# Optimization experiments

Measured on AMD Instinct MI355X. Metric: run time of the kernel, lower is better.

Reference implementation:

```python
import jax, jax.numpy as jnp
import numpy as np
from jax.scipy.linalg import solve_triangular
from jax.scipy.special import logsumexp

N, K, D = 131072, 32, 32
LOG_2PI = np.float32(np.log(2.0 * np.pi))


def setup_inputs() -> dict:
    key = jax.random.key(0)
    k1, k2, k3, k4 = jax.random.split(key, 4)
    X = jax.random.normal(k1, (N, D), dtype=jnp.float32)
    means = jax.random.normal(k2, (K, D), dtype=jnp.float32)
    chols = jax.random.normal(k3, (K, D, D), dtype=jnp.float32)
    weights = jax.random.normal(k4, (K,), dtype=jnp.float32) - 1.0  # normal_(-1, 1)
    return {"X": X, "means": means, "chols": chols, "weights": weights, "it": 0}


def _neglog_likelihood(X, means, chols, weights):
    d = X.shape[-1]
    n = X.shape[0]
    eye = jnp.eye(d, dtype=X.dtype)
    # sigmas[k] = chols[k] @ chols[k]^T + I  -> (K, D, D)
    sigmas = jnp.einsum('kij,klj->kil', chols, chols) + eye
    L = jnp.linalg.cholesky(sigmas)                      # (K, D, D)
    # per-cluster Gaussian log-densities for all points, batched
    diff = X[None, :, :] - means[:, None, :]             # (K, N, D)
    y = solve_triangular(L, diff.transpose(0, 2, 1), lower=True)  # (K, D, N)
    maha = jnp.sum(y * y, axis=1)                        # (K, N)
    logdet = 2.0 * jnp.sum(jnp.log(jnp.diagonal(L, axis1=-2, axis2=-1)), axis=-1)  # (K,)
    log_dens = -0.5 * (maha + (logdet + d * LOG_2PI)[:, None])    # (K, N)
    dens = jnp.exp(log_dens)                             # (K, N)
    # sum_{i,j} w_i w_j N_i(x) N_j(x) = (sum_k w_k N_k(x))^2
    numer = jnp.square(weights @ dens)                   # (N,)
    # pairwise normaliser Z_ij = N(mu_i; mu_j, S_i + S_j), all pairs batched
    S_ij = sigmas[:, None] + sigmas[None, :]             # (K, K, D, D)
    L_ij = jnp.linalg.cholesky(S_ij)
    dmu = means[:, None, :] - means[None, :, :]          # (K, K, D)
    y_ij = solve_triangular(L_ij, dmu[..., None], lower=True)[..., 0]  # (K, K, D)
    maha_ij = jnp.sum(y_ij * y_ij, axis=-1)              # (K, K)
    logdet_ij = 2.0 * jnp.sum(jnp.log(jnp.diagonal(L_ij, axis1=-2, axis2=-1)), axis=-1)
    Z_ij = jnp.exp(-0.5 * (maha_ij + logdet_ij + d * LOG_2PI))
    z = jnp.sum((weights[:, None] * weights[None, :]) * Z_ij)
    pdf = numer / z                                      # (N,)
    logp = jnp.log(pdf)                                  # (N,)
    return -(logsumexp(logp, axis=0) / n)


def reference(X, means, chols, weights, it):
    return _neglog_likelihood(X, means, chols, weights)
```

## Files before the change

### kernel.cpp

```cpp
#include <hip/hip_runtime.h>
#include <math.h>

#define NPTS  131072
#define NPTB  1024
#define NPRB  256
#define GRID  (NPTB + NPRB)
#define DLOG2PIF 58.8120661f
#define DLOG2PI  58.81206612467475
#define SHIFT 92.0f
#define NEGHALF_LOG2E -0.72134752044f
#define LOG2E 1.44269504089f

typedef __attribute__((ext_vector_type(8)))  short short8;
typedef __attribute__((ext_vector_type(16))) float f32x16;

static __device__ __forceinline__ unsigned bfh(float f) {
  unsigned u = __float_as_uint(f);
  return (u + 0x7FFFu + ((u >> 16) & 1u)) >> 16;
}
static __device__ __forceinline__ float bfhf(float f) {
  return __uint_as_float(bfh(f) << 16);
}

__global__ __launch_bounds__(256) void setup_kernel(
    const float* __restrict__ means, const float* __restrict__ chols,
    const float* __restrict__ wts,
    uint4* __restrict__ Afrag, float* __restrict__ gbuf,
    float* __restrict__ Kc, float* __restrict__ Sg,
    unsigned* __restrict__ ticket)
{
  const int tid = threadIdx.x, wv = tid >> 6, lane = tid & 63;
  const int r = lane & 31, h = lane >> 5;
  const int k = blockIdx.x*4 + wv;
  __shared__ float SshA[4][1056];
  float* Ssh = SshA[wv];
  if (blockIdx.x == 0 && tid == 0) *ticket = 0u;
  const float* cp = chols + (size_t)k*1024 + r*32;
  float4 fa = *(const float4*)(cp + h*8);
  float4 fb = *(const float4*)(cp + h*8 + 4);
  float4 fc = *(const float4*)(cp + 16 + h*8);
  float4 fd = *(const float4*)(cp + 16 + h*8 + 4);
  float v0[8] = {fa.x,fa.y,fa.z,fa.w,fb.x,fb.y,fb.z,fb.w};
  float v1[8] = {fc.x,fc.y,fc.z,fc.w,fd.x,fd.y,fd.z,fd.w};
  short8 hi0, hi1, lo0, lo1;
  #pragma unroll
  for (int j = 0; j < 8; j++) {
    hi0[j] = (short)bfh(v0[j]);  lo0[j] = (short)bfh(v0[j] - bfhf(v0[j]));
    hi1[j] = (short)bfh(v1[j]);  lo1[j] = (short)bfh(v1[j] - bfhf(v1[j]));
  }
  f32x16 acc = {};
  acc = __builtin_amdgcn_mfma_f32_32x32x16_bf16(hi0, hi0, acc, 0,0,0);
  acc = __builtin_amdgcn_mfma_f32_32x32x16_bf16(hi1, hi1, acc, 0,0,0);
  acc = __builtin_amdgcn_mfma_f32_32x32x16_bf16(hi0, lo0, acc, 0,0,0);
  acc = __builtin_amdgcn_mfma_f32_32x32x16_bf16(hi1, lo1, acc, 0,0,0);
  acc = __builtin_amdgcn_mfma_f32_32x32x16_bf16(lo0, hi0, acc, 0,0,0);
  acc = __builtin_amdgcn_mfma_f32_32x32x16_bf16(lo1, hi1, acc, 0,0,0);
  #pragma unroll
  for (int q = 0; q < 16; q++) {
    int row = (q & 3) + 8*(q >> 2) + 4*h;
    Ssh[row*33 + r] = acc[q] + ((row == r) ? 1.0f : 0.0f);
  }
  float a[32];
  #pragma unroll
  for (int j = 0; j < 32; j++) a[j] = Ssh[r*33 + j];
  float ldsum = 0.0f;
  #pragma unroll
  for (int j = 0; j < 32; j++) {
    float dd = __shfl(a[j], j);
    float inv = rsqrtf(dd);
    float sq = dd * inv;
    ldsum += __logf(sq);
    float l = a[j] * inv;
    #pragma unroll
    for (int e = j+1; e < 32; e++) {
      float le = __shfl(l, e);
      a[e] = (r >= e) ? fmaf(-l, le, a[e]) : a[e];
    }
    a[j] = (r == j) ? sq : ((r > j) ? l : a[j]);
  }
  #pragma unroll
  for (int j = 0; j < 32; j++) Ssh[r*33 + j] = a[j];
  float bv[32];
  #pragma unroll
  for (int d = 0; d < 32; d++) {
    float s0 = (d == r) ? 1.0f : 0.0f, s1 = 0.0f;
    #pragma unroll
    for (int j = 0; j + 1 < d; j += 2) {
      s0 = fmaf(-Ssh[d*33 + j],     bv[j],   s0);
      s1 = fmaf(-Ssh[d*33 + j + 1], bv[j+1], s1);
    }
    if (d & 1) s0 = fmaf(-Ssh[d*33 + (d-1)], bv[d-1], s0);
    bv[d] = __fdividef(s0 + s1, Ssh[d*33 + d]);
  }
  #pragma unroll
  for (int d = 0; d < 32; d++) Ssh[d*33 + r] = bv[d];
  float t0[8], t1[8];
  #pragma unroll
  for (int j = 0; j < 8; j++) {
    t0[j] = Ssh[r*33 + h*8 + j];
    t1[j] = Ssh[r*33 + 16 + h*8 + j];
  }
  uint4 s0 = make_uint4(bfh(t0[0])|(bfh(t0[1])<<16), bfh(t0[2])|(bfh(t0[3])<<16),
                        bfh(t0[4])|(bfh(t0[5])<<16), bfh(t0[6])|(bfh(t0[7])<<16));
  uint4 s1 = make_uint4(bfh(t1[0])|(bfh(t1[1])<<16), bfh(t1[2])|(bfh(t1[3])<<16),
                        bfh(t1[4])|(bfh(t1[5])<<16), bfh(t1[6])|(bfh(t1[7])<<16));
  Afrag[(k*2 + 0)*64 + lane] = s0;
  Afrag[(k*2 + 1)*64 + lane] = s1;
  const float* mk = means + k*32;
  float wr = 0.0f;
  #pragma unroll
  for (int j = 0; j < 32; j++) wr = fmaf(bfhf(Ssh[r*33 + j]), mk[j], wr);
  float c = wr*wr;
  #pragma unroll
  for (int off = 16; off > 0; off >>= 1) c += __shfl_xor(c, off);
  float gd = 0.0f;
  #pragma unroll
  for (int rr = 0; rr < 32; rr++)
    gd = fmaf(bfhf(bv[rr]), __shfl(wr, rr), gd);
  if (h == 0) gbuf[k*32 + r] = 2.0f*gd;
  if (lane == 0) {
    float wk = wts[k];
    float ld2 = 2.0f*ldsum + DLOG2PIF;
    Kc[k] = LOG2E*(SHIFT - 0.5f*ld2 - 0.5f*c) + log2f(fabsf(wk));
    Sg[k] = (wk < 0.0f) ? -1.0f : 1.0f;
  }
}

__global__ __launch_bounds__(256, 4) void work_kernel(
    const float* __restrict__ X, const float* __restrict__ means,
    const float* __restrict__ chols, const float* __restrict__ wts,
    const uint4* __restrict__ Afrag, const float* __restrict__ gbuf,
    const float* __restrict__ Kc, const float* __restrict__ Sg,
    double* __restrict__ zterm, double* __restrict__ partials,
    unsigned* __restrict__ ticket, float* __restrict__ out)
{
  __shared__ __align__(16) char smem[16896];
  __shared__ float K2sh[32], sksh[32];
  __shared__ double redd[4], redz[4];
  __shared__ unsigned lastFlag;
  const int tid = threadIdx.x, wv = tid >> 6, lane = tid & 63;
  const int r = lane & 31, h = lane >> 5;
  if (blockIdx.x < NPTB) {
    uint4* fsh = (uint4*)smem;
    if (tid < 32) { K2sh[tid] = Kc[tid]; sksh[tid] = Sg[tid]; }
    const int n0 = blockIdx.x*128 + wv*32 + r;
    short8 xh0, xh1;
    {
      const float* xp = X + (size_t)n0*32;
      float4 fa = *(const float4*)(xp + h*8);
      float4 fb = *(const float4*)(xp + h*8 + 4);
      float4 fc = *(const float4*)(xp + 16 + h*8);
      float4 fd = *(const float4*)(xp + 16 + h*8 + 4);
      float v0[8] = {fa.x,fa.y,fa.z,fa.w,fb.x,fb.y,fb.z,fb.w};
      float v1[8] = {fc.x,fc.y,fc.z,fc.w,fd.x,fd.y,fd.z,fd.w};
      #pragma unroll
      for (int j = 0; j < 8; j++) { xh0[j] = (short)bfh(v0[j]); xh1[j] = (short)bfh(v1[j]); }
    }
    f32x16 accg = {};
    {
      const float* gp = gbuf + r*32 + h*8;
      float4 ga = *(const float4*)(gp);
      float4 gb = *(const float4*)(gp + 4);
      float4 gc = *(const float4*)(gp + 16);
      float4 gd = *(const float4*)(gp + 20);
      float g0[8] = {ga.x,ga.y,ga.z,ga.w,gb.x,gb.y,gb.z,gb.w};
      float g1[8] = {gc.x,gc.y,gc.z,gc.w,gd.x,gd.y,gd.z,gd.w};
      short8 Gh0, Gl0, Gh1, Gl1;
      #pragma unroll
      for (int j = 0; j < 8; j++) {
        Gh0[j] = (short)bfh(g0[j]); Gl0[j] = (short)bfh(g0[j] - bfhf(g0[j]));
        Gh1[j] = (short)bfh(g1[j]); Gl1[j] = (short)bfh(g1[j] - bfhf(g1[j]));
      }
      accg = __builtin_amdgcn_mfma_f32_32x32x16_bf16(Gh0, xh0, accg, 0,0,0);
      accg = __builtin_amdgcn_mfma_f32_32x32x16_bf16(Gl0, xh0, accg, 0,0,0);
      accg = __builtin_amdgcn_mfma_f32_32x32x16_bf16(Gh1, xh1, accg, 0,0,0);
      accg = __builtin_amdgcn_mfma_f32_32x32x16_bf16(Gl1, xh1, accg, 0,0,0);
    }
    float sF = 0.0f;
    #pragma unroll
    for (int ph = 0; ph < 4; ph++) {
      __syncthreads();
      {
        const uint4* src = Afrag + ph*1024;
        uint4 t0 = src[tid], t1 = src[tid+256], t2 = src[tid+512], t3 = src[tid+768];
        fsh[tid] = t0; fsh[tid+256] = t1; fsh[tid+512] = t2; fsh[tid+768] = t3;
      }
      __syncthreads();
      const short8* cp0 = (const short8*)fsh;
      short8 c0 = cp0[lane], c1 = cp0[64 + lane];
      #pragma unroll
      for (int kk = 0; kk < 8; kk++) {
        short8 nf0, nf1;
        if (kk < 7) {
          const short8* np = (const short8*)(fsh + (kk+1)*128);
          nf0 = np[lane]; nf1 = np[64 + lane];
        }
        const int kidx = ph*8 + kk;
        const float Kk = K2sh[kidx], sk = sksh[kidx];
        f32x16 acc2 = {};
        acc2 = __builtin_amdgcn_mfma_f32_32x32x16_bf16(c0, xh0, acc2, 0,0,0);
        acc2 = __builtin_amdgcn_mfma_f32_32x32x16_bf16(c1, xh1, acc2, 0,0,0);
        float ma = 0.f, mb = 0.f;
        #pragma unroll
        for (int q = 0; q < 8; q++) {
          ma = fmaf(acc2[q],   acc2[q],   ma);
          mb = fmaf(acc2[q+8], acc2[q+8], mb);
        }
        const int qg = (kidx & 3) | (((kidx >> 3) & 3) << 2);
        const int hneed = (kidx >> 2) & 1;
        float m = ma + mb - ((h == hneed) ? accg[qg] : 0.0f);
        m += __shfl_xor(m, 32);
        sF = fmaf(sk, exp2f(fmaf(m, NEGHALF_LOG2E, Kk)), sF);
        c0 = nf0; c1 = nf1;
      }
    }
    double Tp = (double)sF*(double)sF;
    if (lane >= 32) Tp = 0.0;
    #pragma unroll
    for (int off = 32; off > 0; off >>= 1) Tp += __shfl_down(Tp, off);
    if (lane == 0) redd[wv] = Tp;
    __syncthreads();
    if (tid == 0) partials[blockIdx.x] = redd[0] + redd[1] + redd[2] + redd[3];
  } else {
    float* Ssh = (float*)smem + wv*1056;
    const int pid = (blockIdx.x - NPTB)*4 + wv, pi = pid >> 5, pj = pid & 31;
    const float* cpi = chols + (size_t)pi*1024 + r*32;
    const float* cpj = chols + (size_t)pj*1024 + r*32;
    float4 ia = *(const float4*)(cpi + h*8);
    float4 ib = *(const float4*)(cpi + h*8 + 4);
    float4 ic = *(const float4*)(cpi + 16 + h*8);
    float4 id = *(const float4*)(cpi + 16 + h*8 + 4);
    float4 ja = *(const float4*)(cpj + h*8);
    float4 jb = *(const float4*)(cpj + h*8 + 4);
    float4 jc = *(const float4*)(cpj + 16 + h*8);
    float4 jd = *(const float4*)(cpj + 16 + h*8 + 4);
    float vi0[8] = {ia.x,ia.y,ia.z,ia.w,ib.x,ib.y,ib.z,ib.w};
    float vi1[8] = {ic.x,ic.y,ic.z,ic.w,id.x,id.y,id.z,id.w};
    float vj0[8] = {ja.x,ja.y,ja.z,ja.w,jb.x,jb.y,jb.z,jb.w};
    float vj1[8] = {jc.x,jc.y,jc.z,jc.w,jd.x,jd.y,jd.z,jd.w};
    short8 I0h,I0l,I1h,I1l,J0h,J0l,J1h,J1l;
    #pragma unroll
    for (int j = 0; j < 8; j++) {
      I0h[j]=(short)bfh(vi0[j]); I0l[j]=(short)bfh(vi0[j]-bfhf(vi0[j]));
      I1h[j]=(short)bfh(vi1[j]); I1l[j]=(short)bfh(vi1[j]-bfhf(vi1[j]));
      J0h[j]=(short)bfh(vj0[j]); J0l[j]=(short)bfh(vj0[j]-bfhf(vj0[j]));
      J1h[j]=(short)bfh(vj1[j]); J1l[j]=(short)bfh(vj1[j]-bfhf(vj1[j]));
    }
    f32x16 pacc = {};
    pacc = __builtin_amdgcn_mfma_f32_32x32x16_bf16(I0h, I0h, pacc, 0,0,0);
    pacc = __builtin_amdgcn_mfma_f32_32x32x16_bf16(I1h, I1h, pacc, 0,0,0);
    pacc = __builtin_amdgcn_mfma_f32_32x32x16_bf16(I0h, I0l, pacc, 0,0,0);
    pacc = __builtin_amdgcn_mfma_f32_32x32x16_bf16(I1h, I1l, pacc, 0,0,0);
    pacc = __builtin_amdgcn_mfma_f32_32x32x16_bf16(I0l, I0h, pacc, 0,0,0);
    pacc = __builtin_amdgcn_mfma_f32_32x32x16_bf16(I1l, I1h, pacc, 0,0,0);
    pacc = __builtin_amdgcn_mfma_f32_32x32x16_bf16(J0h, J0h, pacc, 0,0,0);
    pacc = __builtin_amdgcn_mfma_f32_32x32x16_bf16(J1h, J1h, pacc, 0,0,0);
    pacc = __builtin_amdgcn_mfma_f32_32x32x16_bf16(J0h, J0l, pacc, 0,0,0);
    pacc = __builtin_amdgcn_mfma_f32_32x32x16_bf16(J1h, J1l, pacc, 0,0,0);
    pacc = __builtin_amdgcn_mfma_f32_32x32x16_bf16(J0l, J0h, pacc, 0,0,0);
    pacc = __builtin_amdgcn_mfma_f32_32x32x16_bf16(J1l, J1h, pacc, 0,0,0);
    #pragma unroll
    for (int q = 0; q < 16; q++) {
      int row = (q & 3) + 8*(q >> 2) + 4*h;
      Ssh[row*33 + r] = pacc[q] + ((row == r) ? 2.0f : 0.0f);
    }
    float a[32];
    #pragma unroll
    for (int j = 0; j < 32; j++) a[j] = Ssh[r*33 + j];
    #pragma unroll
    for (int j = 0; j < 32; j++) {
      float dd = __shfl(a[j], j);
      float inv = __frsqrt_rn(dd);
      float sq = dd * inv;
      float l = a[j] * inv;
      #pragma unroll
      for (int e = j+1; e < 32; e++) {
        float le = __shfl(l, e);
        a[e] = (r >= e) ? fmaf(-l, le, a[e]) : a[e];
      }
      a[j] = (r == j) ? sq : ((r > j) ? l : a[j]);
    }
    float acc2 = means[pi*32 + r] - means[pj*32 + r];
    float maha = 0.0f, ldsum = 0.0f;
    #pragma unroll
    for (int d = 0; d < 32; d++) {
      float dd = __shfl(a[d], d);
      float yd = __shfl(acc2, d) / dd;
      maha = fmaf(yd, yd, maha);
      ldsum += __logf(dd);
      acc2 = (r > d) ? fmaf(-a[d], yd, acc2) : acc2;
    }
    if (lane == 0) {
      double vd = -0.5 * ((double)maha + 2.0*(double)ldsum + DLOG2PI);
      zterm[pid] = (double)wts[pi] * (double)wts[pj] * exp(vd);
    }
  }
  __syncthreads();
  if (tid == 0) {
    __threadfence();
    lastFlag = (atomicAdd(ticket, 1u) == GRID - 1) ? 1u : 0u;
  }
  __syncthreads();
  if (lastFlag) {
    __threadfence();
    double t = 0.0, z = 0.0;
    for (int p = tid; p < NPTB; p += 256) t += partials[p];
    for (int p = tid; p < 1024; p += 256) z += zterm[p];
    #pragma unroll
    for (int off = 32; off > 0; off >>= 1) {
      t += __shfl_down(t, off);
      z += __shfl_down(z, off);
    }
    if (lane == 0) { redd[wv] = t; redz[wv] = z; }
    __syncthreads();
    if (tid == 0) {
      t = redd[0] + redd[1] + redd[2] + redd[3];
      z = redz[0] + redz[1] + redz[2] + redz[3];
      double logT = log(t) - 2.0*(double)SHIFT;
      double logz = log(z);
      out[0] = (float)((logz - logT) / (double)NPTS);
    }
  }
}

extern "C" void kernel_launch(void* const* d_in, const int* in_sizes, int n_in,
                              void* d_out, int out_size, void* d_ws, size_t ws_size,
                              hipStream_t stream) {
  const float* X     = (const float*)d_in[0];
  const float* means = (const float*)d_in[1];
  const float* chols = (const float*)d_in[2];
  const float* wts   = (const float*)d_in[3];
  float* out = (float*)d_out;
  char* ws = (char*)d_ws;
  uint4*    Afrag    = (uint4*)ws;
  float*    gbuf     = (float*)(ws + 65536);
  float*    Kc       = (float*)(ws + 69632);
  float*    Sg       = (float*)(ws + 69760);
  double*   zterm    = (double*)(ws + 69888);
  double*   partials = (double*)(ws + 78080);
  unsigned* ticket   = (unsigned*)(ws + 86272);

  setup_kernel<<<8, 256, 0, stream>>>(means, chols, wts, Afrag, gbuf, Kc, Sg, ticket);
  work_kernel<<<GRID, 256, 0, stream>>>(X, means, chols, wts, Afrag, gbuf, Kc, Sg,
                                        zterm, partials, ticket, out);
}
```

Baseline: 131.5 us.

## Move pairwise normaliser to setup kernel and process two point tiles per wave

```diff
diff --git a/kernel.cpp b/kernel.cpp
--- a/kernel.cpp
+++ b/kernel.cpp
@@ -2,9 +2,9 @@
 #include <math.h>
 
 #define NPTS  131072
-#define NPTB  1024
+#define NPTB  512
 #define NPRB  256
-#define GRID  (NPTB + NPRB)
+#define GRIDW NPTB
 #define DLOG2PIF 58.8120661f
 #define DLOG2PI  58.81206612467475
 #define SHIFT 92.0f
@@ -27,203 +27,106 @@
     const float* __restrict__ wts,
     uint4* __restrict__ Afrag, float* __restrict__ gbuf,
     float* __restrict__ Kc, float* __restrict__ Sg,
-    unsigned* __restrict__ ticket)
+    double* __restrict__ zterm, unsigned* __restrict__ ticket)
 {
   const int tid = threadIdx.x, wv = tid >> 6, lane = tid & 63;
   const int r = lane & 31, h = lane >> 5;
-  const int k = blockIdx.x*4 + wv;
   __shared__ float SshA[4][1056];
   float* Ssh = SshA[wv];
-  if (blockIdx.x == 0 && tid == 0) *ticket = 0u;
-  const float* cp = chols + (size_t)k*1024 + r*32;
-  float4 fa = *(const float4*)(cp + h*8);
-  float4 fb = *(const float4*)(cp + h*8 + 4);
-  float4 fc = *(const float4*)(cp + 16 + h*8);
-  float4 fd = *(const float4*)(cp + 16 + h*8 + 4);
-  float v0[8] = {fa.x,fa.y,fa.z,fa.w,fb.x,fb.y,fb.z,fb.w};
-  float v1[8] = {fc.x,fc.y,fc.z,fc.w,fd.x,fd.y,fd.z,fd.w};
-  short8 hi0, hi1, lo0, lo1;
-  #pragma unroll
-  for (int j = 0; j < 8; j++) {
-    hi0[j] = (short)bfh(v0[j]);  lo0[j] = (short)bfh(v0[j] - bfhf(v0[j]));
-    hi1[j] = (short)bfh(v1[j]);  lo1[j] = (short)bfh(v1[j] - bfhf(v1[j]));
-  }
-  f32x16 acc = {};
-  acc = __builtin_amdgcn_mfma_f32_32x32x16_bf16(hi0, hi0, acc, 0,0,0);
-  acc = __builtin_amdgcn_mfma_f32_32x32x16_bf16(hi1, hi1, acc, 0,0,0);
-  acc = __builtin_amdgcn_mfma_f32_32x32x16_bf16(hi0, lo0, acc, 0,0,0);
-  acc = __builtin_amdgcn_mfma_f32_32x32x16_bf16(hi1, lo1, acc, 0,0,0);
-  acc = __builtin_amdgcn_mfma_f32_32x32x16_bf16(lo0, hi0, acc, 0,0,0);
-  acc = __builtin_amdgcn_mfma_f32_32x32x16_bf16(lo1, hi1, acc, 0,0,0);
-  #pragma unroll
-  for (int q = 0; q < 16; q++) {
-    int row = (q & 3) + 8*(q >> 2) + 4*h;
-    Ssh[row*33 + r] = acc[q] + ((row == r) ? 1.0f : 0.0f);
-  }
-  float a[32];
-  #pragma unroll
-  for (int j = 0; j < 32; j++) a[j] = Ssh[r*33 + j];
-  float ldsum = 0.0f;
-  #pragma unroll
-  for (int j = 0; j < 32; j++) {
-    float dd = __shfl(a[j], j);
-    float inv = rsqrtf(dd);
-    float sq = dd * inv;
-    ldsum += __logf(sq);
-    float l = a[j] * inv;
-    #pragma unroll
-    for (int e = j+1; e < 32; e++) {
-      float le = __shfl(l, e);
-      a[e] = (r >= e) ? fmaf(-l, le, a[e]) : a[e];
-    }
-    a[j] = (r == j) ? sq : ((r > j) ? l : a[j]);
-  }
-  #pragma unroll
-  for (int j = 0; j < 32; j++) Ssh[r*33 + j] = a[j];
-  float bv[32];
-  #pragma unroll
-  for (int d = 0; d < 32; d++) {
-    float s0 = (d == r) ? 1.0f : 0.0f, s1 = 0.0f;
-    #pragma unroll
-    for (int j = 0; j + 1 < d; j += 2) {
-      s0 = fmaf(-Ssh[d*33 + j],     bv[j],   s0);
-      s1 = fmaf(-Ssh[d*33 + j + 1], bv[j+1], s1);
-    }
-    if (d & 1) s0 = fmaf(-Ssh[d*33 + (d-1)], bv[d-1], s0);
-    bv[d] = __fdividef(s0 + s1, Ssh[d*33 + d]);
-  }
-  #pragma unroll
-  for (int d = 0; d < 32; d++) Ssh[d*33 + r] = bv[d];
-  float t0[8], t1[8];
-  #pragma unroll
-  for (int j = 0; j < 8; j++) {
-    t0[j] = Ssh[r*33 + h*8 + j];
-    t1[j] = Ssh[r*33 + 16 + h*8 + j];
-  }
-  uint4 s0 = make_uint4(bfh(t0[0])|(bfh(t0[1])<<16), bfh(t0[2])|(bfh(t0[3])<<16),
-                        bfh(t0[4])|(bfh(t0[5])<<16), bfh(t0[6])|(bfh(t0[7])<<16));
-  uint4 s1 = make_uint4(bfh(t1[0])|(bfh(t1[1])<<16), bfh(t1[2])|(bfh(t1[3])<<16),
-                        bfh(t1[4])|(bfh(t1[5])<<16), bfh(t1[6])|(bfh(t1[7])<<16));
-  Afrag[(k*2 + 0)*64 + lane] = s0;
-  Afrag[(k*2 + 1)*64 + lane] = s1;
-  const float* mk = means + k*32;
-  float wr = 0.0f;
-  #pragma unroll
-  for (int j = 0; j < 32; j++) wr = fmaf(bfhf(Ssh[r*33 + j]), mk[j], wr);
-  float c = wr*wr;
-  #pragma unroll
-  for (int off = 16; off > 0; off >>= 1) c += __shfl_xor(c, off);
-  float gd = 0.0f;
-  #pragma unroll
-  for (int rr = 0; rr < 32; rr++)
-    gd = fmaf(bfhf(bv[rr]), __shfl(wr, rr), gd);
-  if (h == 0) gbuf[k*32 + r] = 2.0f*gd;
-  if (lane == 0) {
-    float wk = wts[k];
-    float ld2 = 2.0f*ldsum + DLOG2PIF;
-    Kc[k] = LOG2E*(SHIFT - 0.5f*ld2 - 0.5f*c) + log2f(fabsf(wk));
-    Sg[k] = (wk < 0.0f) ? -1.0f : 1.0f;
-  }
-}
-
-__global__ __launch_bounds__(256, 4) void work_kernel(
-    const float* __restrict__ X, const float* __restrict__ means,
-    const float* __restrict__ chols, const float* __restrict__ wts,
-    const uint4* __restrict__ Afrag, const float* __restrict__ gbuf,
-    const float* __restrict__ Kc, const float* __restrict__ Sg,
-    double* __restrict__ zterm, double* __restrict__ partials,
-    unsigned* __restrict__ ticket, float* __restrict__ out)
-{
-  __shared__ __align__(16) char smem[16896];
-  __shared__ float K2sh[32], sksh[32];
-  __shared__ double redd[4], redz[4];
-  __shared__ unsigned lastFlag;
-  const int tid = threadIdx.x, wv = tid >> 6, lane = tid & 63;
-  const int r = lane & 31, h = lane >> 5;
-  if (blockIdx.x < NPTB) {
-    uint4* fsh = (uint4*)smem;
-    if (tid < 32) { K2sh[tid] = Kc[tid]; sksh[tid] = Sg[tid]; }
-    const int n0 = blockIdx.x*128 + wv*32 + r;
-    short8 xh0, xh1;
-    {
-      const float* xp = X + (size_t)n0*32;
-      float4 fa = *(const float4*)(xp + h*8);
-      float4 fb = *(const float4*)(xp + h*8 + 4);
-      float4 fc = *(const float4*)(xp + 16 + h*8);
-      float4 fd = *(const float4*)(xp + 16 + h*8 + 4);
-      float v0[8] = {fa.x,fa.y,fa.z,fa.w,fb.x,fb.y,fb.z,fb.w};
-      float v1[8] = {fc.x,fc.y,fc.z,fc.w,fd.x,fd.y,fd.z,fd.w};
+  if (blockIdx.x < 8) {
+    const int k = blockIdx.x*4 + wv;
+    if (blockIdx.x == 0 && tid == 0) *ticket = 0u;
+    const float* cp = chols + (size_t)k*1024 + r*32;
+    float4 fa = *(const float4*)(cp + h*8);
+    float4 fb = *(const float4*)(cp + h*8 + 4);
+    float4 fc = *(const float4*)(cp + 16 + h*8);
+    float4 fd = *(const float4*)(cp + 16 + h*8 + 4);
+    float v0[8] = {fa.x,fa.y,fa.z,fa.w,fb.x,fb.y,fb.z,fb.w};
+    float v1[8] = {fc.x,fc.y,fc.z,fc.w,fd.x,fd.y,fd.z,fd.w};
+    short8 hi0, hi1, lo0, lo1;
+    #pragma unroll
+    for (int j = 0; j < 8; j++) {
+      hi0[j] = (short)bfh(v0[j]);  lo0[j] = (short)bfh(v0[j] - bfhf(v0[j]));
+      hi1[j] = (short)bfh(v1[j]);  lo1[j] = (short)bfh(v1[j] - bfhf(v1[j]));
+    }
+    f32x16 acc = {};
+    acc = __builtin_amdgcn_mfma_f32_32x32x16_bf16(hi0, hi0, acc, 0,0,0);
+    acc = __builtin_amdgcn_mfma_f32_32x32x16_bf16(hi1, hi1, acc, 0,0,0);
+    acc = __builtin_amdgcn_mfma_f32_32x32x16_bf16(hi0, lo0, acc, 0,0,0);
+    acc = __builtin_amdgcn_mfma_f32_32x32x16_bf16(hi1, lo1, acc, 0,0,0);
+    acc = __builtin_amdgcn_mfma_f32_32x32x16_bf16(lo0, hi0, acc, 0,0,0);
+    acc = __builtin_amdgcn_mfma_f32_32x32x16_bf16(lo1, hi1, acc, 0,0,0);
+    #pragma unroll
+    for (int q = 0; q < 16; q++) {
+      int row = (q & 3) + 8*(q >> 2) + 4*h;
+      Ssh[row*33 + r] = acc[q] + ((row == r) ? 1.0f : 0.0f);
+    }
+    float a[32];
+    #pragma unroll
+    for (int j = 0; j < 32; j++) a[j] = Ssh[r*33 + j];
+    float ldsum = 0.0f;
+    #pragma unroll
+    for (int j = 0; j < 32; j++) {
+      float dd = __shfl(a[j], j);
+      float inv = rsqrtf(dd);
+      float sq = dd * inv;
+      ldsum += __logf(sq);
+      float l = a[j] * inv;
       #pragma unroll
-      for (int j = 0; j < 8; j++) { xh0[j] = (short)bfh(v0[j]); xh1[j] = (short)bfh(v1[j]); }
-    }
-    f32x16 accg = {};
-    {
-      const float* gp = gbuf + r*32 + h*8;
-      float4 ga = *(const float4*)(gp);
-      float4 gb = *(const float4*)(gp + 4);
-      float4 gc = *(const float4*)(gp + 16);
-      float4 gd = *(const float4*)(gp + 20);
-      float g0[8] = {ga.x,ga.y,ga.z,ga.w,gb.x,gb.y,gb.z,gb.w};
-      float g1[8] = {gc.x,gc.y,gc.z,gc.w,gd.x,gd.y,gd.z,gd.w};
-      short8 Gh0, Gl0, Gh1, Gl1;
+      for (int e = j+1; e < 32; e++) {
+        float le = __shfl(l, e);
+        a[e] = (r >= e) ? fmaf(-l, le, a[e]) : a[e];
+      }
+      a[j] = (r == j) ? sq : ((r > j) ? l : a[j]);
+    }
+    #pragma unroll
+    for (int j = 0; j < 32; j++) Ssh[r*33 + j] = a[j];
+    float bv[32];
+    #pragma unroll
+    for (int d = 0; d < 32; d++) {
+      float s0 = (d == r) ? 1.0f : 0.0f, s1 = 0.0f;
       #pragma unroll
-      for (int j = 0; j < 8; j++) {
-        Gh0[j] = (short)bfh(g0[j]); Gl0[j] = (short)bfh(g0[j] - bfhf(g0[j]));
-        Gh1[j] = (short)bfh(g1[j]); Gl1[j] = (short)bfh(g1[j] - bfhf(g1[j]));
+      for (int j = 0; j + 1 < d; j += 2) {
+        s0 = fmaf(-Ssh[d*33 + j],     bv[j],   s0);
+        s1 = fmaf(-Ssh[d*33 + j + 1], bv[j+1], s1);
       }
-      accg = __builtin_amdgcn_mfma_f32_32x32x16_bf16(Gh0, xh0, accg, 0,0,0);
-      accg = __builtin_amdgcn_mfma_f32_32x32x16_bf16(Gl0, xh0, accg, 0,0,0);
-      accg = __builtin_amdgcn_mfma_f32_32x32x16_bf16(Gh1, xh1, accg, 0,0,0);
-      accg = __builtin_amdgcn_mfma_f32_32x32x16_bf16(Gl1, xh1, accg, 0,0,0);
-    }
-    float sF = 0.0f;
-    #pragma unroll
-    for (int ph = 0; ph < 4; ph++) {
-      __syncthreads();
-      {
-        const uint4* src = Afrag + ph*1024;
-        uint4 t0 = src[tid], t1 = src[tid+256], t2 = src[tid+512], t3 = src[tid+768];
-        fsh[tid] = t0; fsh[tid+256] = t1; fsh[tid+512] = t2; fsh[tid+768] = t3;
-      }
-      __syncthreads();
-      const short8* cp0 = (const short8*)fsh;
-      short8 c0 = cp0[lane], c1 = cp0[64 + lane];
-      #pragma unroll
-      for (int kk = 0; kk < 8; kk++) {
-        short8 nf0, nf1;
-        if (kk < 7) {
-          const short8* np = (const short8*)(fsh + (kk+1)*128);
-          nf0 = np[lane]; nf1 = np[64 + lane];
-        }
-        const int kidx = ph*8 + kk;
-        const float Kk = K2sh[kidx], sk = sksh[kidx];
-        f32x16 acc2 = {};
-        acc2 = __builtin_amdgcn_mfma_f32_32x32x16_bf16(c0, xh0, acc2, 0,0,0);
-        acc2 = __builtin_amdgcn_mfma_f32_32x32x16_bf16(c1, xh1, acc2, 0,0,0);
-        float ma = 0.f, mb = 0.f;
-        #pragma unroll
-        for (int q = 0; q < 8; q++) {
-          ma = fmaf(acc2[q],   acc2[q],   ma);
-          mb = fmaf(acc2[q+8], acc2[q+8], mb);
-        }
-        const int qg = (kidx & 3) | (((kidx >> 3) & 3) << 2);
-        const int hneed = (kidx >> 2) & 1;
-        float m = ma + mb - ((h == hneed) ? accg[qg] : 0.0f);
-        m += __shfl_xor(m, 32);
-        sF = fmaf(sk, exp2f(fmaf(m, NEGHALF_LOG2E, Kk)), sF);
-        c0 = nf0; c1 = nf1;
-      }
-    }
-    double Tp = (double)sF*(double)sF;
-    if (lane >= 32) Tp = 0.0;
-    #pragma unroll
-    for (int off = 32; off > 0; off >>= 1) Tp += __shfl_down(Tp, off);
-    if (lane == 0) redd[wv] = Tp;
-    __syncthreads();
-    if (tid == 0) partials[blockIdx.x] = redd[0] + redd[1] + redd[2] + redd[3];
+      if (d & 1) s0 = fmaf(-Ssh[d*33 + (d-1)], bv[d-1], s0);
+      bv[d] = __fdividef(s0 + s1, Ssh[d*33 + d]);
+    }
+    #pragma unroll
+    for (int d = 0; d < 32; d++) Ssh[d*33 + r] = bv[d];
+    float t0[8], t1[8];
+    #pragma unroll
+    for (int j = 0; j < 8; j++) {
+      t0[j] = Ssh[r*33 + h*8 + j];
+      t1[j] = Ssh[r*33 + 16 + h*8 + j];
+    }
+    uint4 s0 = make_uint4(bfh(t0[0])|(bfh(t0[1])<<16), bfh(t0[2])|(bfh(t0[3])<<16),
+                          bfh(t0[4])|(bfh(t0[5])<<16), bfh(t0[6])|(bfh(t0[7])<<16));
+    uint4 s1 = make_uint4(bfh(t1[0])|(bfh(t1[1])<<16), bfh(t1[2])|(bfh(t1[3])<<16),
+                          bfh(t1[4])|(bfh(t1[5])<<16), bfh(t1[6])|(bfh(t1[7])<<16));
+    Afrag[(k*2 + 0)*64 + lane] = s0;
+    Afrag[(k*2 + 1)*64 + lane] = s1;
+    const float* mk = means + k*32;
+    float wr = 0.0f;
+    #pragma unroll
+    for (int j = 0; j < 32; j++) wr = fmaf(bfhf(Ssh[r*33 + j]), mk[j], wr);
+    float c = wr*wr;
+    #pragma unroll
+    for (int off = 16; off > 0; off >>= 1) c += __shfl_xor(c, off);
+    float gd = 0.0f;
+    #pragma unroll
+    for (int rr = 0; rr < 32; rr++)
+      gd = fmaf(bfhf(bv[rr]), __shfl(wr, rr), gd);
+    if (h == 0) gbuf[k*32 + r] = 2.0f*gd;
+    if (lane == 0) {
+      float wk = wts[k];
+      float ld2 = 2.0f*ldsum + DLOG2PIF;
+      Kc[k] = LOG2E*(SHIFT - 0.5f*ld2 - 0.5f*c) + log2f(fabsf(wk));
+      Sg[k] = (wk < 0.0f) ? -1.0f : 1.0f;
+    }
   } else {
-    float* Ssh = (float*)smem + wv*1056;
-    const int pid = (blockIdx.x - NPTB)*4 + wv, pi = pid >> 5, pj = pid & 31;
+    const int pid = (blockIdx.x - 8)*4 + wv, pi = pid >> 5, pj = pid & 31;
     const float* cpi = chols + (size_t)pi*1024 + r*32;
     const float* cpj = chols + (size_t)pj*1024 + r*32;
     float4 ia = *(const float4*)(cpi + h*8);
@@ -295,10 +198,120 @@
       zterm[pid] = (double)wts[pi] * (double)wts[pj] * exp(vd);
     }
   }
+}
+
+__global__ __launch_bounds__(256) void work_kernel(
+    const float* __restrict__ X,
+    const uint4* __restrict__ Afrag, const float* __restrict__ gbuf,
+    const float* __restrict__ Kc, const float* __restrict__ Sg,
+    const double* __restrict__ zterm, double* __restrict__ partials,
+    unsigned* __restrict__ ticket, float* __restrict__ out)
+{
+  __shared__ float K2sh[32], sksh[32];
+  __shared__ double redd[4], redz[4];
+  __shared__ unsigned lastFlag;
+  const int tid = threadIdx.x, wv = tid >> 6, lane = tid & 63;
+  const int r = lane & 31, h = lane >> 5;
+  if (tid < 32) { K2sh[tid] = Kc[tid]; sksh[tid] = Sg[tid]; }
+  const int n0 = blockIdx.x*256 + wv*64 + r;
+  short8 xh00, xh01, xh10, xh11;
+  {
+    const float* xp0 = X + (size_t)n0*32;
+    const float* xp1 = X + (size_t)(n0+32)*32;
+    float4 fa = *(const float4*)(xp0 + h*8);
+    float4 fb = *(const float4*)(xp0 + h*8 + 4);
+    float4 fc = *(const float4*)(xp0 + 16 + h*8);
+    float4 fd = *(const float4*)(xp0 + 16 + h*8 + 4);
+    float4 ga = *(const float4*)(xp1 + h*8);
+    float4 gb = *(const float4*)(xp1 + h*8 + 4);
+    float4 gc = *(const float4*)(xp1 + 16 + h*8);
+    float4 gd = *(const float4*)(xp1 + 16 + h*8 + 4);
+    float v00[8] = {fa.x,fa.y,fa.z,fa.w,fb.x,fb.y,fb.z,fb.w};
+    float v01[8] = {fc.x,fc.y,fc.z,fc.w,fd.x,fd.y,fd.z,fd.w};
+    float v10[8] = {ga.x,ga.y,ga.z,ga.w,gb.x,gb.y,gb.z,gb.w};
+    float v11[8] = {gc.x,gc.y,gc.z,gc.w,gd.x,gd.y,gd.z,gd.w};
+    #pragma unroll
+    for (int j = 0; j < 8; j++) {
+      xh00[j] = (short)bfh(v00[j]);  xh01[j] = (short)bfh(v01[j]);
+      xh10[j] = (short)bfh(v10[j]);  xh11[j] = (short)bfh(v11[j]);
+    }
+  }
+  __syncthreads();
+  f32x16 accg0 = {}, accg1 = {};
+  {
+    const float* gp = gbuf + r*32 + h*8;
+    float4 ga = *(const float4*)(gp);
+    float4 gb = *(const float4*)(gp + 4);
+    float4 gc = *(const float4*)(gp + 16);
+    float4 gd = *(const float4*)(gp + 20);
+    float g0[8] = {ga.x,ga.y,ga.z,ga.w,gb.x,gb.y,gb.z,gb.w};
+    float g1[8] = {gc.x,gc.y,gc.z,gc.w,gd.x,gd.y,gd.z,gd.w};
+    short8 Gh0, Gl0, Gh1, Gl1;
+    #pragma unroll
+    for (int j = 0; j < 8; j++) {
+      Gh0[j] = (short)bfh(g0[j]); Gl0[j] = (short)bfh(g0[j] - bfhf(g0[j]));
+      Gh1[j] = (short)bfh(g1[j]); Gl1[j] = (short)bfh(g1[j] - bfhf(g1[j]));
+    }
+    accg0 = __builtin_amdgcn_mfma_f32_32x32x16_bf16(Gh0, xh00, accg0, 0,0,0);
+    accg0 = __builtin_amdgcn_mfma_f32_32x32x16_bf16(Gl0, xh00, accg0, 0,0,0);
+    accg0 = __builtin_amdgcn_mfma_f32_32x32x16_bf16(Gh1, xh01, accg0, 0,0,0);
+    accg0 = __builtin_amdgcn_mfma_f32_32x32x16_bf16(Gl1, xh01, accg0, 0,0,0);
+    accg1 = __builtin_amdgcn_mfma_f32_32x32x16_bf16(Gh0, xh10, accg1, 0,0,0);
+    accg1 = __builtin_amdgcn_mfma_f32_32x32x16_bf16(Gl0, xh10, accg1, 0,0,0);
+    accg1 = __builtin_amdgcn_mfma_f32_32x32x16_bf16(Gh1, xh11, accg1, 0,0,0);
+    accg1 = __builtin_amdgcn_mfma_f32_32x32x16_bf16(Gl1, xh11, accg1, 0,0,0);
+  }
+  const short8* ab = (const short8*)Afrag + lane;
+  short8 fA0 = ab[0*128], fA1 = ab[0*128 + 64];
+  short8 fB0 = ab[1*128], fB1 = ab[1*128 + 64];
+  float sF0 = 0.0f, sF1 = 0.0f;
+  #pragma unroll
+  for (int kk = 0; kk < 32; kk++) {
+    short8 c0, c1;
+    if ((kk & 1) == 0) { c0 = fA0; c1 = fA1; } else { c0 = fB0; c1 = fB1; }
+    if (kk + 2 < 32) {
+      if ((kk & 1) == 0) { fA0 = ab[(kk+2)*128]; fA1 = ab[(kk+2)*128 + 64]; }
+      else               { fB0 = ab[(kk+2)*128]; fB1 = ab[(kk+2)*128 + 64]; }
+    }
+    const float Kk = K2sh[kk], sk = sksh[kk];
+    f32x16 acc0 = {}, acc1 = {};
+    acc0 = __builtin_amdgcn_mfma_f32_32x32x16_bf16(c0, xh00, acc0, 0,0,0);
+    acc0 = __builtin_amdgcn_mfma_f32_32x32x16_bf16(c1, xh01, acc0, 0,0,0);
+    acc1 = __builtin_amdgcn_mfma_f32_32x32x16_bf16(c0, xh10, acc1, 0,0,0);
+    acc1 = __builtin_amdgcn_mfma_f32_32x32x16_bf16(c1, xh11, acc1, 0,0,0);
+    float m0a=0.f, m0b=0.f, m0c=0.f, m0d=0.f;
+    float m1a=0.f, m1b=0.f, m1c=0.f, m1d=0.f;
+    #pragma unroll
+    for (int q = 0; q < 4; q++) {
+      m0a = fmaf(acc0[q],    acc0[q],    m0a);
+      m0b = fmaf(acc0[q+4],  acc0[q+4],  m0b);
+      m0c = fmaf(acc0[q+8],  acc0[q+8],  m0c);
+      m0d = fmaf(acc0[q+12], acc0[q+12], m0d);
+      m1a = fmaf(acc1[q],    acc1[q],    m1a);
+      m1b = fmaf(acc1[q+4],  acc1[q+4],  m1b);
+      m1c = fmaf(acc1[q+8],  acc1[q+8],  m1c);
+      m1d = fmaf(acc1[q+12], acc1[q+12], m1d);
+    }
+    const int qg = (kk & 3) | (((kk >> 3) & 3) << 2);
+    const int hneed = (kk >> 2) & 1;
+    float m0 = (m0a + m0b) + (m0c + m0d) - ((h == hneed) ? accg0[qg] : 0.0f);
+    float m1 = (m1a + m1b) + (m1c + m1d) - ((h == hneed) ? accg1[qg] : 0.0f);
+    m0 += __shfl_xor(m0, 32);
+    m1 += __shfl_xor(m1, 32);
+    sF0 = fmaf(sk, exp2f(fmaf(m0, NEGHALF_LOG2E, Kk)), sF0);
+    sF1 = fmaf(sk, exp2f(fmaf(m1, NEGHALF_LOG2E, Kk)), sF1);
+  }
+  double Tp = (double)sF0*(double)sF0 + (double)sF1*(double)sF1;
+  if (lane >= 32) Tp = 0.0;
+  #pragma unroll
+  for (int off = 32; off > 0; off >>= 1) Tp += __shfl_down(Tp, off);
+  if (lane == 0) redd[wv] = Tp;
+  __syncthreads();
+  if (tid == 0) partials[blockIdx.x] = redd[0] + redd[1] + redd[2] + redd[3];
   __syncthreads();
   if (tid == 0) {
     __threadfence();
-    lastFlag = (atomicAdd(ticket, 1u) == GRID - 1) ? 1u : 0u;
+    lastFlag = (atomicAdd(ticket, 1u) == GRIDW - 1) ? 1u : 0u;
   }
   __syncthreads();
   if (lastFlag) {
@@ -338,9 +351,10 @@
   float*    Sg       = (float*)(ws + 69760);
   double*   zterm    = (double*)(ws + 69888);
   double*   partials = (double*)(ws + 78080);
-  unsigned* ticket   = (unsigned*)(ws + 86272);
-
-  setup_kernel<<<8, 256, 0, stream>>>(means, chols, wts, Afrag, gbuf, Kc, Sg, ticket);
-  work_kernel<<<GRID, 256, 0, stream>>>(X, means, chols, wts, Afrag, gbuf, Kc, Sg,
-                                        zterm, partials, ticket, out);
-}
+  unsigned* ticket   = (unsigned*)(ws + 82176);
+
+  setup_kernel<<<8 + NPRB, 256, 0, stream>>>(means, chols, wts, Afrag, gbuf,
+                                             Kc, Sg, zterm, ticket);
+  work_kernel<<<GRIDW, 256, 0, stream>>>(X, Afrag, gbuf, Kc, Sg,
+                                         zterm, partials, ticket, out);
+}
```

Measured after the change: 117.1 us. 1.12x faster.
